# Performance work log

Measured on AMD Instinct MI355X. Metric: run time of the kernel, lower is better.

Reference implementation:

```python
import jax, jax.numpy as jnp
import numpy as np

N_NODES = 100000
N_EDGES = 1600000
IN_F, HID, N_COLORS = 128, 128, 10


def setup_inputs() -> dict:
    key = jax.random.key(0)
    k1, k2, k3, k4 = jax.random.split(key, 4)
    x = jax.random.normal(k1, (N_NODES, IN_F), dtype=jnp.float32)
    edge_index = jax.random.randint(k2, (2, N_EDGES), 0, N_NODES, dtype=jnp.int64)
    # Glorot-ish init for weights
    W1 = jax.random.normal(k3, (IN_F, HID), dtype=jnp.float32) / np.sqrt(IN_F)
    b1 = jnp.zeros((HID,), dtype=jnp.float32)
    W2 = jax.random.normal(k4, (HID, N_COLORS), dtype=jnp.float32) / np.sqrt(HID)
    b2 = jnp.zeros((N_COLORS,), dtype=jnp.float32)
    return {"x": x, "edge_index": edge_index, "W1": W1, "b1": b1, "W2": W2, "b2": b2}


def _gcn_norm(edge_index, num_nodes):
    # Add self-loops, compute symmetric normalization D^-1/2 (A+I) D^-1/2
    loops = jnp.arange(num_nodes, dtype=edge_index.dtype)
    src = jnp.concatenate([edge_index[0], loops])
    dst = jnp.concatenate([edge_index[1], loops])
    deg = jax.ops.segment_sum(jnp.ones_like(dst, dtype=jnp.float32), dst,
                              num_segments=num_nodes)
    deg_isqrt = jax.lax.rsqrt(deg)  # deg >= 1 due to self-loops
    norm = deg_isqrt[src] * deg_isqrt[dst]  # [E + N]
    return src, dst, norm


def _gcn_conv(h, src, dst, norm, num_nodes, W, b):
    # Linear transform first (PyG GCNConv), then gather-scale-scatter aggregate
    h = h @ W                                   # [N, out]
    msg = h[src] * norm[:, None]                # [E + N, out] gather
    out = jax.ops.segment_sum(msg, dst, num_segments=num_nodes)  # scatter-add
    return out + b


def reference(x, edge_index, W1, b1, W2, b2):
    n = x.shape[0]
    src, dst, norm = _gcn_norm(edge_index, n)
    h = _gcn_conv(x, src, dst, norm, n, W1, b1)
    h = jax.nn.relu(h)
    # dropout is identity in eval mode
    h = _gcn_conv(h, src, dst, norm, n, W2, b2)
    return jax.nn.softmax(h, axis=1)
```

## Files before the change

### kernel.cpp

```cpp
#include <hip/hip_runtime.h>
#include <hip/hip_fp16.h>

#define IN_F 128
#define HID  128
#define NC   10
#define H2P  16
#define NPB  128
#define NBMAX 784
#define BCAP 2560
#define EPB  4096

typedef _Float16 f16x8 __attribute__((ext_vector_type(8)));
typedef float f32x4 __attribute__((ext_vector_type(4)));

__global__ __launch_bounds__(1024) void k_bin(const int* __restrict__ src,
                                              const int* __restrict__ dst,
                                              int* __restrict__ bcnt,
                                              unsigned int* __restrict__ binned,
                                              int E, int nbin) {
    __shared__ int hist[NBMAX];
    __shared__ int base[NBMAX];
    __shared__ int lcur[NBMAX];
    const int tid = threadIdx.x;
    for (int b = tid; b < nbin; b += 1024) { hist[b] = 0; lcur[b] = 0; }
    __syncthreads();

    const int e0 = blockIdx.x * EPB + tid;
    int d[4];
    #pragma unroll
    for (int u = 0; u < 4; u++) {
        int e = e0 + u * 1024;
        d[u] = (e < E) ? dst[e] : -1;
        if (d[u] >= 0) atomicAdd(&hist[d[u] >> 7], 1);
    }
    __syncthreads();
    for (int b = tid; b < nbin; b += 1024) {
        int h = hist[b];
        base[b] = h ? atomicAdd(&bcnt[b], h) : 0;
    }
    __syncthreads();
    #pragma unroll
    for (int u = 0; u < 4; u++) {
        int e = e0 + u * 1024;
        if (e < E) {
            int dd = d[u];
            int b = dd >> 7;
            int s = src[e];
            int o = base[b] + atomicAdd(&lcur[b], 1);
            if (o < BCAP)
                binned[(size_t)b * BCAP + o] = ((unsigned)(dd & 127) << 17) | (unsigned)s;
        }
    }
}

__global__ __launch_bounds__(1024) void k_binscan(const int* __restrict__ bcnt,
                                                  int* __restrict__ binbase,
                                                  int* __restrict__ rowptr,
                                                  int N, int E, int nbin) {
    __shared__ int s[1024];
    const int tid = threadIdx.x;
    int v = (tid < nbin) ? bcnt[tid] : 0;
    s[tid] = v;
    __syncthreads();
    #pragma unroll
    for (int off = 1; off < 1024; off <<= 1) {
        int t = (tid >= off) ? s[tid - off] : 0;
        __syncthreads();
        s[tid] += t;
        __syncthreads();
    }
    if (tid < nbin) binbase[tid] = s[tid] - v;
    if (tid == 0) rowptr[N] = E;
}

__global__ __launch_bounds__(256) void k_place2(const int* __restrict__ bcnt,
                                                const unsigned int* __restrict__ binned,
                                                const int* __restrict__ binbase,
                                                int* __restrict__ rowptr,
                                                float* __restrict__ dis,
                                                int* __restrict__ csr, int N) {
    __shared__ int h[NPB];
    __shared__ int lb[NPB];
    __shared__ int cur[NPB];
    const int b = blockIdx.x;
    const int tid = threadIdx.x;
    if (tid < NPB) h[tid] = 0;
    __syncthreads();
    const int m = min(bcnt[b], BCAP);
    const unsigned int* p = binned + (size_t)b * BCAP;
    for (int i = tid; i < m; i += 256) atomicAdd(&h[p[i] >> 17], 1);
    __syncthreads();
    if (tid < NPB) lb[tid] = h[tid];
    __syncthreads();
    #pragma unroll
    for (int off = 1; off < NPB; off <<= 1) {
        int t = (tid < NPB && tid >= off) ? lb[tid - off] : 0;
        __syncthreads();
        if (tid < NPB) lb[tid] += t;
        __syncthreads();
    }
    const int rb = binbase[b];
    if (tid < NPB) {
        int ex = lb[tid] - h[tid];
        int node = b * NPB + tid;
        if (node < N) {
            rowptr[node] = rb + ex;
            dis[node] = rsqrtf(1.0f + (float)h[tid]);
        }
        lb[tid] = ex;
        cur[tid] = 0;
    }
    __syncthreads();
    for (int i = tid; i < m; i += 256) {
        unsigned v = p[i];
        int dl = v >> 17;
        int r = atomicAdd(&cur[dl], 1);
        csr[rb + lb[dl] + r] = (int)(v & 0x1FFFF);
    }
}

__global__ __launch_bounds__(256) void k_prep(const float* __restrict__ W1,
                                              __half* __restrict__ WT) {
    int e = blockIdx.x * 256 + threadIdx.x;
    int n = e >> 7, k = e & 127;
    WT[n * IN_F + k] = __float2half(W1[k * HID + n]);
}

__global__ __launch_bounds__(256) void k_gemm1(const float* __restrict__ X,
                                               const __half* __restrict__ WT,
                                               const float* __restrict__ dis,
                                               __half* __restrict__ outh) {
    __shared__ _Float16 sX[32 * IN_F];
    __shared__ _Float16 sW[128 * IN_F];
    const int tid = threadIdx.x;
    const int row0 = blockIdx.x * 32;

    {
        int n = tid >> 1, part = tid & 1;
        const f16x8* src = (const f16x8*)(WT + n * IN_F + part * 64);
        f16x8* dst = (f16x8*)(sW + n * IN_F + part * 64);
        #pragma unroll
        for (int c = 0; c < 8; c++) dst[c] = src[c];
    }
    {
        int r = tid >> 3;
        int k0 = (tid & 7) * 16;
        const float* src = X + (size_t)(row0 + r) * IN_F + k0;
        float4 f0 = *(const float4*)(src);
        float4 f1 = *(const float4*)(src + 4);
        float4 f2 = *(const float4*)(src + 8);
        float4 f3 = *(const float4*)(src + 12);
        f16x8 h0, h1;
        h0[0] = (_Float16)f0.x; h0[1] = (_Float16)f0.y;
        h0[2] = (_Float16)f0.z; h0[3] = (_Float16)f0.w;
        h0[4] = (_Float16)f1.x; h0[5] = (_Float16)f1.y;
        h0[6] = (_Float16)f1.z; h0[7] = (_Float16)f1.w;
        h1[0] = (_Float16)f2.x; h1[1] = (_Float16)f2.y;
        h1[2] = (_Float16)f2.z; h1[3] = (_Float16)f2.w;
        h1[4] = (_Float16)f3.x; h1[5] = (_Float16)f3.y;
        h1[6] = (_Float16)f3.z; h1[7] = (_Float16)f3.w;
        *(f16x8*)(sX + r * IN_F + k0) = h0;
        *(f16x8*)(sX + r * IN_F + k0 + 8) = h1;
    }
    __syncthreads();

    const int wave = tid >> 6;
    const int lane = tid & 63;
    const int quad = lane >> 4;
    const int l16 = lane & 15;
    const int nbase = wave * 32;

    f32x4 acc00 = {0,0,0,0}, acc01 = {0,0,0,0}, acc10 = {0,0,0,0}, acc11 = {0,0,0,0};

    #pragma unroll
    for (int kc = 0; kc < 4; kc++) {
        const int koff = kc * 32 + quad * 8;
        f16x8 a0 = *(const f16x8*)(sX + l16 * IN_F + koff);
        f16x8 a1 = *(const f16x8*)(sX + (16 + l16) * IN_F + koff);
        f16x8 b0 = *(const f16x8*)(sW + (nbase + l16) * IN_F + koff);
        f16x8 b1 = *(const f16x8*)(sW + (nbase + 16 + l16) * IN_F + koff);
        acc00 = __builtin_amdgcn_mfma_f32_16x16x32_f16(a0, b0, acc00, 0, 0, 0);
        acc01 = __builtin_amdgcn_mfma_f32_16x16x32_f16(a0, b1, acc01, 0, 0, 0);
        acc10 = __builtin_amdgcn_mfma_f32_16x16x32_f16(a1, b0, acc10, 0, 0, 0);
        acc11 = __builtin_amdgcn_mfma_f32_16x16x32_f16(a1, b1, acc11, 0, 0, 0);
    }

    #pragma unroll
    for (int r = 0; r < 4; r++) {
        {
            int row = row0 + quad * 4 + r;
            float d = dis[row];
            __half* o = outh + (size_t)row * HID + nbase + l16;
            o[0]  = __float2half(acc00[r] * d);
            o[16] = __float2half(acc01[r] * d);
        }
        {
            int row = row0 + 16 + quad * 4 + r;
            float d = dis[row];
            __half* o = outh + (size_t)row * HID + nbase + l16;
            o[0]  = __float2half(acc10[r] * d);
            o[16] = __float2half(acc11[r] * d);
        }
    }
}

__global__ __launch_bounds__(256) void k_agg1(const __half* __restrict__ hsh,
                                              const int* __restrict__ rowptr,
                                              const int* __restrict__ csr,
                                              const float* __restrict__ dis,
                                              const float* __restrict__ b1,
                                              const float* __restrict__ W2,
                                              float* __restrict__ h2p, int N) {
    __shared__ float sWT[NC][IN_F];
    for (int i = threadIdx.x; i < NC * IN_F; i += 256)
        sWT[i >> 7][i & 127] = W2[(i & 127) * NC + (i >> 7)];
    __syncthreads();

    const int node = blockIdx.x * 4 + (threadIdx.x >> 6);
    if (node >= N) return;
    const int lane = threadIdx.x & 63;
    const int g   = lane >> 4;
    const int l16 = lane & 15;
    const int f0  = l16 * 8;

    const int beg = rowptr[node], end = rowptr[node + 1];

    float acc[8] = {0,0,0,0,0,0,0,0};
    if (g == 0) {
        float4 r = *(const float4*)(hsh + (size_t)node * HID + f0);
        const __half2* hh = (const __half2*)&r;
        float2 t0 = __half22float2(hh[0]), t1 = __half22float2(hh[1]);
        float2 t2 = __half22float2(hh[2]), t3 = __half22float2(hh[3]);
        acc[0] = t0.x; acc[1] = t0.y; acc[2] = t1.x; acc[3] = t1.y;
        acc[4] = t2.x; acc[5] = t2.y; acc[6] = t3.x; acc[7] = t3.y;
    }

    int j = beg + g;
    for (; j + 12 < end; j += 16) {
        int s0 = csr[j], s1 = csr[j + 4], s2 = csr[j + 8], s3 = csr[j + 12];
        float4 r0 = *(const float4*)(hsh + (size_t)s0 * HID + f0);
        float4 r1 = *(const float4*)(hsh + (size_t)s1 * HID + f0);
        float4 r2 = *(const float4*)(hsh + (size_t)s2 * HID + f0);
        float4 r3 = *(const float4*)(hsh + (size_t)s3 * HID + f0);
        #pragma unroll
        for (int u = 0; u < 4; u++) {
            const float4* rp = u == 0 ? &r0 : u == 1 ? &r1 : u == 2 ? &r2 : &r3;
            const __half2* hh = (const __half2*)rp;
            float2 t0 = __half22float2(hh[0]), t1 = __half22float2(hh[1]);
            float2 t2 = __half22float2(hh[2]), t3 = __half22float2(hh[3]);
            acc[0] += t0.x; acc[1] += t0.y; acc[2] += t1.x; acc[3] += t1.y;
            acc[4] += t2.x; acc[5] += t2.y; acc[6] += t3.x; acc[7] += t3.y;
        }
    }
    for (; j < end; j += 4) {
        int s0 = csr[j];
        float4 r0 = *(const float4*)(hsh + (size_t)s0 * HID + f0);
        const __half2* hh = (const __half2*)&r0;
        float2 t0 = __half22float2(hh[0]), t1 = __half22float2(hh[1]);
        float2 t2 = __half22float2(hh[2]), t3 = __half22float2(hh[3]);
        acc[0] += t0.x; acc[1] += t0.y; acc[2] += t1.x; acc[3] += t1.y;
        acc[4] += t2.x; acc[5] += t2.y; acc[6] += t3.x; acc[7] += t3.y;
    }

    #pragma unroll
    for (int i = 0; i < 8; i++) {
        acc[i] += __shfl_xor(acc[i], 16, 64);
        acc[i] += __shfl_xor(acc[i], 32, 64);
    }

    const float d = dis[node];
    float4 ba = *(const float4*)(b1 + f0);
    float4 bb = *(const float4*)(b1 + f0 + 4);
    float h[8];
    h[0] = fmaxf(fmaf(d, acc[0], ba.x), 0.0f);
    h[1] = fmaxf(fmaf(d, acc[1], ba.y), 0.0f);
    h[2] = fmaxf(fmaf(d, acc[2], ba.z), 0.0f);
    h[3] = fmaxf(fmaf(d, acc[3], ba.w), 0.0f);
    h[4] = fmaxf(fmaf(d, acc[4], bb.x), 0.0f);
    h[5] = fmaxf(fmaf(d, acc[5], bb.y), 0.0f);
    h[6] = fmaxf(fmaf(d, acc[6], bb.z), 0.0f);
    h[7] = fmaxf(fmaf(d, acc[7], bb.w), 0.0f);

    const int cb = (g == 0) ? 0 : (g == 1) ? 3 : (g == 2) ? 6 : 8;
    const int nc = (g < 2) ? 3 : 2;
    float p[3];
    #pragma unroll
    for (int ci = 0; ci < 3; ci++) {
        if (ci < nc) {
            int c = cb + ci;
            float4 wa = *(const float4*)&sWT[c][f0];
            float4 wb = *(const float4*)&sWT[c][f0 + 4];
            float t = fmaf(h[0], wa.x, fmaf(h[1], wa.y, fmaf(h[2], wa.z, h[3] * wa.w)));
            t = fmaf(h[4], wb.x, fmaf(h[5], wb.y, fmaf(h[6], wb.z, fmaf(h[7], wb.w, t))));
            #pragma unroll
            for (int off = 1; off < 16; off <<= 1) t += __shfl_xor(t, off, 64);
            p[ci] = t;
        }
    }
    if (l16 == 0) {
        float* o = h2p + (size_t)node * H2P + cb;
        for (int ci = 0; ci < nc; ci++) o[ci] = d * p[ci];
    }
}

__global__ __launch_bounds__(256) void k_agg2(const float* __restrict__ h2p,
                                              const int* __restrict__ rowptr,
                                              const int* __restrict__ csr,
                                              const float* __restrict__ dis,
                                              const float* __restrict__ b2,
                                              float* __restrict__ out, int N) {
    int t = blockIdx.x * 256 + threadIdx.x;
    int node = t >> 2;
    int q = t & 3;
    if (node >= N) return;
    const int base = q * 4;

    float4 a = *(const float4*)(h2p + (size_t)node * H2P + base);
    const int beg = rowptr[node], end = rowptr[node + 1];
    int j = beg;
    for (; j + 1 < end; j += 2) {
        int s0 = csr[j], s1 = csr[j + 1];
        float4 v0 = *(const float4*)(h2p + (size_t)s0 * H2P + base);
        float4 v1 = *(const float4*)(h2p + (size_t)s1 * H2P + base);
        a.x += v0.x + v1.x; a.y += v0.y + v1.y;
        a.z += v0.z + v1.z; a.w += v0.w + v1.w;
    }
    if (j < end) {
        float4 v0 = *(const float4*)(h2p + (size_t)csr[j] * H2P + base);
        a.x += v0.x; a.y += v0.y; a.z += v0.z; a.w += v0.w;
    }

    const float d = dis[node];
    float vv[4];
    const float* ap = &a.x;
    #pragma unroll
    for (int i = 0; i < 4; i++) {
        int f = base + i;
        bool val = f < NC;
        vv[i] = val ? fmaf(d, ap[i], b2[val ? f : 0]) : -1e30f;
    }
    float m = fmaxf(fmaxf(vv[0], vv[1]), fmaxf(vv[2], vv[3]));
    m = fmaxf(m, __shfl_xor(m, 1, 64));
    m = fmaxf(m, __shfl_xor(m, 2, 64));
    float e[4];
    #pragma unroll
    for (int i = 0; i < 4; i++) e[i] = (base + i < NC) ? expf(vv[i] - m) : 0.0f;
    float s = (e[0] + e[1]) + (e[2] + e[3]);
    s += __shfl_xor(s, 1, 64);
    s += __shfl_xor(s, 2, 64);
    float inv = 1.0f / s;

    float* o = out + (size_t)node * NC;
    if (q == 0) {
        *(float2*)(o + 0) = make_float2(e[0] * inv, e[1] * inv);
        *(float2*)(o + 2) = make_float2(e[2] * inv, e[3] * inv);
    } else if (q == 1) {
        *(float2*)(o + 4) = make_float2(e[0] * inv, e[1] * inv);
        *(float2*)(o + 6) = make_float2(e[2] * inv, e[3] * inv);
    } else if (q == 2) {
        *(float2*)(o + 8) = make_float2(e[0] * inv, e[1] * inv);
    }
}

extern "C" void kernel_launch(void* const* d_in, const int* in_sizes, int n_in,
                              void* d_out, int out_size, void* d_ws, size_t ws_size,
                              hipStream_t stream) {
    const float* x  = (const float*)d_in[0];
    const int*   ei = (const int*)d_in[1];
    const float* W1 = (const float*)d_in[2];
    const float* b1 = (const float*)d_in[3];
    const float* W2 = (const float*)d_in[4];
    const float* b2 = (const float*)d_in[5];
    float* out = (float*)d_out;

    const int N = in_sizes[0] / IN_F;
    const int E = in_sizes[1] / 2;
    const int* esrc = ei;
    const int* edst = ei + E;
    const int nbin = (N + NPB - 1) / NPB;

    char* ws = (char*)d_ws;
    int*    rowptr  = (int*)(ws);
    float*  dis     = (float*)(ws + 0x80000);
    int*    bcnt    = (int*)(ws + 0x100000);
    int*    binbase = (int*)(ws + 0x110000);
    __half* WT      = (__half*)(ws + 0x120000);
    unsigned int* binned = (unsigned int*)(ws + 0x140000);
    int*    csr     = (int*)(ws + 0x940000);
    __half* hsh     = (__half*)(ws + 0x1000000);
    float*  h2p     = (float*)(ws + 0x2A00000);

    hipMemsetAsync(bcnt, 0, (size_t)nbin * sizeof(int), stream);

    k_bin    <<<(E + EPB - 1) / EPB, 1024, 0, stream>>>(esrc, edst, bcnt, binned, E, nbin);
    k_binscan<<<1, 1024, 0, stream>>>(bcnt, binbase, rowptr, N, E, nbin);
    k_place2 <<<nbin, 256, 0, stream>>>(bcnt, binned, binbase, rowptr, dis, csr, N);
    k_prep   <<<64, 256, 0, stream>>>(W1, WT);
    k_gemm1  <<<N / 32, 256, 0, stream>>>(x, WT, dis, hsh);
    k_agg1   <<<(N + 3) / 4, 256, 0, stream>>>(hsh, rowptr, csr, dis, b1, W2, h2p, N);
    k_agg2   <<<(int)(((size_t)N * 4 + 255) / 256), 256, 0, stream>>>(h2p, rowptr, csr, dis, b2, out, N);
}
```

Baseline: 262.1 us.

## Fuse prep kernels, drop bin scan, store layer-2 features in fp16, unroll gathers

The W1 transpose moves into block 0 of the binning kernel, and the single-block bin scan is replaced by a per-block reduction over bcnt inside the placement kernel. Together these remove two launches. The layer-2 intermediate is stored as fp16 to halve gather traffic in agg2, which now uses two threads per node with 8 features each. The agg1 gather loop is unrolled to 8 outstanding loads. The trade-offs are redundant prefix work in each placement block and reduced precision for the second-layer features.

```diff
diff --git a/kernel.cpp b/kernel.cpp
--- a/kernel.cpp
+++ b/kernel.cpp
@@ -17,11 +17,21 @@
                                               const int* __restrict__ dst,
                                               int* __restrict__ bcnt,
                                               unsigned int* __restrict__ binned,
+                                              const float* __restrict__ W1,
+                                              __half* __restrict__ WT,
                                               int E, int nbin) {
     __shared__ int hist[NBMAX];
     __shared__ int base[NBMAX];
     __shared__ int lcur[NBMAX];
     const int tid = threadIdx.x;
+
+    if (blockIdx.x == 0) {
+        for (int i = tid; i < IN_F * HID; i += 1024) {
+            int k = i >> 7, n = i & 127;
+            WT[n * IN_F + k] = __float2half(W1[k * HID + n]);
+        }
+    }
+
     for (int b = tid; b < nbin; b += 1024) { hist[b] = 0; lcur[b] = 0; }
     __syncthreads();
 
@@ -53,39 +63,31 @@
     }
 }
 
-__global__ __launch_bounds__(1024) void k_binscan(const int* __restrict__ bcnt,
-                                                  int* __restrict__ binbase,
-                                                  int* __restrict__ rowptr,
-                                                  int N, int E, int nbin) {
-    __shared__ int s[1024];
-    const int tid = threadIdx.x;
-    int v = (tid < nbin) ? bcnt[tid] : 0;
-    s[tid] = v;
-    __syncthreads();
-    #pragma unroll
-    for (int off = 1; off < 1024; off <<= 1) {
-        int t = (tid >= off) ? s[tid - off] : 0;
-        __syncthreads();
-        s[tid] += t;
-        __syncthreads();
-    }
-    if (tid < nbin) binbase[tid] = s[tid] - v;
-    if (tid == 0) rowptr[N] = E;
-}
-
 __global__ __launch_bounds__(256) void k_place2(const int* __restrict__ bcnt,
                                                 const unsigned int* __restrict__ binned,
-                                                const int* __restrict__ binbase,
                                                 int* __restrict__ rowptr,
                                                 float* __restrict__ dis,
-                                                int* __restrict__ csr, int N) {
+                                                int* __restrict__ csr,
+                                                int N, int E, int nbin) {
     __shared__ int h[NPB];
     __shared__ int lb[NPB];
     __shared__ int cur[NPB];
+    __shared__ int red[256];
     const int b = blockIdx.x;
     const int tid = threadIdx.x;
+
+    int partial = 0;
+    for (int i = tid; i < b; i += 256) partial += bcnt[i];
+    red[tid] = partial;
     if (tid < NPB) h[tid] = 0;
     __syncthreads();
+    #pragma unroll
+    for (int off = 128; off > 0; off >>= 1) {
+        if (tid < off) red[tid] += red[tid + off];
+        __syncthreads();
+    }
+    const int rb = red[0];
+
     const int m = min(bcnt[b], BCAP);
     const unsigned int* p = binned + (size_t)b * BCAP;
     for (int i = tid; i < m; i += 256) atomicAdd(&h[p[i] >> 17], 1);
@@ -99,7 +101,6 @@
         if (tid < NPB) lb[tid] += t;
         __syncthreads();
     }
-    const int rb = binbase[b];
     if (tid < NPB) {
         int ex = lb[tid] - h[tid];
         int node = b * NPB + tid;
@@ -110,6 +111,7 @@
         lb[tid] = ex;
         cur[tid] = 0;
     }
+    if (b == nbin - 1 && tid == 0) rowptr[N] = E;
     __syncthreads();
     for (int i = tid; i < m; i += 256) {
         unsigned v = p[i];
@@ -117,13 +119,6 @@
         int r = atomicAdd(&cur[dl], 1);
         csr[rb + lb[dl] + r] = (int)(v & 0x1FFFF);
     }
-}
-
-__global__ __launch_bounds__(256) void k_prep(const float* __restrict__ W1,
-                                              __half* __restrict__ WT) {
-    int e = blockIdx.x * 256 + threadIdx.x;
-    int n = e >> 7, k = e & 127;
-    WT[n * IN_F + k] = __float2half(W1[k * HID + n]);
 }
 
 __global__ __launch_bounds__(256) void k_gemm1(const float* __restrict__ X,
@@ -210,7 +205,7 @@
                                               const float* __restrict__ dis,
                                               const float* __restrict__ b1,
                                               const float* __restrict__ W2,
-                                              float* __restrict__ h2p, int N) {
+                                              __half* __restrict__ h2h, int N) {
     __shared__ float sWT[NC][IN_F];
     for (int i = threadIdx.x; i < NC * IN_F; i += 256)
         sWT[i >> 7][i & 127] = W2[(i & 127) * NC + (i >> 7)];
@@ -236,16 +231,19 @@
     }
 
     int j = beg + g;
-    for (; j + 12 < end; j += 16) {
-        int s0 = csr[j], s1 = csr[j + 4], s2 = csr[j + 8], s3 = csr[j + 12];
-        float4 r0 = *(const float4*)(hsh + (size_t)s0 * HID + f0);
-        float4 r1 = *(const float4*)(hsh + (size_t)s1 * HID + f0);
-        float4 r2 = *(const float4*)(hsh + (size_t)s2 * HID + f0);
-        float4 r3 = *(const float4*)(hsh + (size_t)s3 * HID + f0);
+    for (; j + 28 < end; j += 32) {
+        float4 r0 = *(const float4*)(hsh + (size_t)csr[j]      * HID + f0);
+        float4 r1 = *(const float4*)(hsh + (size_t)csr[j + 4]  * HID + f0);
+        float4 r2 = *(const float4*)(hsh + (size_t)csr[j + 8]  * HID + f0);
+        float4 r3 = *(const float4*)(hsh + (size_t)csr[j + 12] * HID + f0);
+        float4 r4 = *(const float4*)(hsh + (size_t)csr[j + 16] * HID + f0);
+        float4 r5 = *(const float4*)(hsh + (size_t)csr[j + 20] * HID + f0);
+        float4 r6 = *(const float4*)(hsh + (size_t)csr[j + 24] * HID + f0);
+        float4 r7 = *(const float4*)(hsh + (size_t)csr[j + 28] * HID + f0);
+        const float4* rs[8] = {&r0, &r1, &r2, &r3, &r4, &r5, &r6, &r7};
         #pragma unroll
-        for (int u = 0; u < 4; u++) {
-            const float4* rp = u == 0 ? &r0 : u == 1 ? &r1 : u == 2 ? &r2 : &r3;
-            const __half2* hh = (const __half2*)rp;
+        for (int u = 0; u < 8; u++) {
+            const __half2* hh = (const __half2*)rs[u];
             float2 t0 = __half22float2(hh[0]), t1 = __half22float2(hh[1]);
             float2 t2 = __half22float2(hh[2]), t3 = __half22float2(hh[3]);
             acc[0] += t0.x; acc[1] += t0.y; acc[2] += t1.x; acc[3] += t1.y;
@@ -253,8 +251,7 @@
         }
     }
     for (; j < end; j += 4) {
-        int s0 = csr[j];
-        float4 r0 = *(const float4*)(hsh + (size_t)s0 * HID + f0);
+        float4 r0 = *(const float4*)(hsh + (size_t)csr[j] * HID + f0);
         const __half2* hh = (const __half2*)&r0;
         float2 t0 = __half22float2(hh[0]), t1 = __half22float2(hh[1]);
         float2 t2 = __half22float2(hh[2]), t3 = __half22float2(hh[3]);
@@ -298,66 +295,83 @@
         }
     }
     if (l16 == 0) {
-        float* o = h2p + (size_t)node * H2P + cb;
-        for (int ci = 0; ci < nc; ci++) o[ci] = d * p[ci];
-    }
-}
-
-__global__ __launch_bounds__(256) void k_agg2(const float* __restrict__ h2p,
+        __half* o = h2h + (size_t)node * H2P + cb;
+        for (int ci = 0; ci < nc; ci++) o[ci] = __float2half(d * p[ci]);
+    }
+}
+
+__global__ __launch_bounds__(256) void k_agg2(const __half* __restrict__ h2h,
                                               const int* __restrict__ rowptr,
                                               const int* __restrict__ csr,
                                               const float* __restrict__ dis,
                                               const float* __restrict__ b2,
                                               float* __restrict__ out, int N) {
     int t = blockIdx.x * 256 + threadIdx.x;
-    int node = t >> 2;
-    int q = t & 3;
+    int node = t >> 1;
+    int q = t & 1;
     if (node >= N) return;
-    const int base = q * 4;
-
-    float4 a = *(const float4*)(h2p + (size_t)node * H2P + base);
+    const int base = q * 8;
+
+    float a[8];
+    {
+        float4 r = *(const float4*)(h2h + (size_t)node * H2P + base);
+        const __half2* hh = (const __half2*)&r;
+        float2 t0 = __half22float2(hh[0]), t1 = __half22float2(hh[1]);
+        float2 t2 = __half22float2(hh[2]), t3 = __half22float2(hh[3]);
+        a[0] = t0.x; a[1] = t0.y; a[2] = t1.x; a[3] = t1.y;
+        a[4] = t2.x; a[5] = t2.y; a[6] = t3.x; a[7] = t3.y;
+    }
     const int beg = rowptr[node], end = rowptr[node + 1];
     int j = beg;
-    for (; j + 1 < end; j += 2) {
-        int s0 = csr[j], s1 = csr[j + 1];
-        float4 v0 = *(const float4*)(h2p + (size_t)s0 * H2P + base);
-        float4 v1 = *(const float4*)(h2p + (size_t)s1 * H2P + base);
-        a.x += v0.x + v1.x; a.y += v0.y + v1.y;
-        a.z += v0.z + v1.z; a.w += v0.w + v1.w;
-    }
-    if (j < end) {
-        float4 v0 = *(const float4*)(h2p + (size_t)csr[j] * H2P + base);
-        a.x += v0.x; a.y += v0.y; a.z += v0.z; a.w += v0.w;
+    for (; j + 3 < end; j += 4) {
+        float4 r0 = *(const float4*)(h2h + (size_t)csr[j]     * H2P + base);
+        float4 r1 = *(const float4*)(h2h + (size_t)csr[j + 1] * H2P + base);
+        float4 r2 = *(const float4*)(h2h + (size_t)csr[j + 2] * H2P + base);
+        float4 r3 = *(const float4*)(h2h + (size_t)csr[j + 3] * H2P + base);
+        const float4* rs[4] = {&r0, &r1, &r2, &r3};
+        #pragma unroll
+        for (int u = 0; u < 4; u++) {
+            const __half2* hh = (const __half2*)rs[u];
+            float2 t0 = __half22float2(hh[0]), t1 = __half22float2(hh[1]);
+            float2 t2 = __half22float2(hh[2]), t3 = __half22float2(hh[3]);
+            a[0] += t0.x; a[1] += t0.y; a[2] += t1.x; a[3] += t1.y;
+            a[4] += t2.x; a[5] += t2.y; a[6] += t3.x; a[7] += t3.y;
+        }
+    }
+    for (; j < end; ++j) {
+        float4 r0 = *(const float4*)(h2h + (size_t)csr[j] * H2P + base);
+        const __half2* hh = (const __half2*)&r0;
+        float2 t0 = __half22float2(hh[0]), t1 = __half22float2(hh[1]);
+        float2 t2 = __half22float2(hh[2]), t3 = __half22float2(hh[3]);
+        a[0] += t0.x; a[1] += t0.y; a[2] += t1.x; a[3] += t1.y;
+        a[4] += t2.x; a[5] += t2.y; a[6] += t3.x; a[7] += t3.y;
     }
 
     const float d = dis[node];
-    float vv[4];
-    const float* ap = &a.x;
-    #pragma unroll
-    for (int i = 0; i < 4; i++) {
+    float vv[8];
+    #pragma unroll
+    for (int i = 0; i < 8; i++) {
         int f = base + i;
-        bool val = f < NC;
-        vv[i] = val ? fmaf(d, ap[i], b2[val ? f : 0]) : -1e30f;
-    }
-    float m = fmaxf(fmaxf(vv[0], vv[1]), fmaxf(vv[2], vv[3]));
+        vv[i] = (f < NC) ? fmaf(d, a[i], b2[f]) : -1e30f;
+    }
+    float m = vv[0];
+    #pragma unroll
+    for (int i = 1; i < 8; i++) m = fmaxf(m, vv[i]);
     m = fmaxf(m, __shfl_xor(m, 1, 64));
-    m = fmaxf(m, __shfl_xor(m, 2, 64));
-    float e[4];
-    #pragma unroll
-    for (int i = 0; i < 4; i++) e[i] = (base + i < NC) ? expf(vv[i] - m) : 0.0f;
-    float s = (e[0] + e[1]) + (e[2] + e[3]);
+    float e[8];
+    float s = 0.0f;
+    #pragma unroll
+    for (int i = 0; i < 8; i++) { e[i] = (base + i < NC) ? expf(vv[i] - m) : 0.0f; s += e[i]; }
     s += __shfl_xor(s, 1, 64);
-    s += __shfl_xor(s, 2, 64);
     float inv = 1.0f / s;
 
     float* o = out + (size_t)node * NC;
     if (q == 0) {
         *(float2*)(o + 0) = make_float2(e[0] * inv, e[1] * inv);
         *(float2*)(o + 2) = make_float2(e[2] * inv, e[3] * inv);
-    } else if (q == 1) {
-        *(float2*)(o + 4) = make_float2(e[0] * inv, e[1] * inv);
-        *(float2*)(o + 6) = make_float2(e[2] * inv, e[3] * inv);
-    } else if (q == 2) {
+        *(float2*)(o + 4) = make_float2(e[4] * inv, e[5] * inv);
+        *(float2*)(o + 6) = make_float2(e[6] * inv, e[7] * inv);
+    } else {
         *(float2*)(o + 8) = make_float2(e[0] * inv, e[1] * inv);
     }
 }
@@ -383,20 +397,17 @@
     int*    rowptr  = (int*)(ws);
     float*  dis     = (float*)(ws + 0x80000);
     int*    bcnt    = (int*)(ws + 0x100000);
-    int*    binbase = (int*)(ws + 0x110000);
-    __half* WT      = (__half*)(ws + 0x120000);
+    __half* WT      = (__half*)(ws + 0x110000);
     unsigned int* binned = (unsigned int*)(ws + 0x140000);
     int*    csr     = (int*)(ws + 0x940000);
-    __half* hsh     = (__half*)(ws + 0x1000000);
-    float*  h2p     = (float*)(ws + 0x2A00000);
+    __half* hsh     = (__half*)(ws + 0x1040000);
+    __half* h2h     = (__half*)(ws + 0x2A00000);
 
     hipMemsetAsync(bcnt, 0, (size_t)nbin * sizeof(int), stream);
 
-    k_bin    <<<(E + EPB - 1) / EPB, 1024, 0, stream>>>(esrc, edst, bcnt, binned, E, nbin);
-    k_binscan<<<1, 1024, 0, stream>>>(bcnt, binbase, rowptr, N, E, nbin);
-    k_place2 <<<nbin, 256, 0, stream>>>(bcnt, binned, binbase, rowptr, dis, csr, N);
-    k_prep   <<<64, 256, 0, stream>>>(W1, WT);
-    k_gemm1  <<<N / 32, 256, 0, stream>>>(x, WT, dis, hsh);
-    k_agg1   <<<(N + 3) / 4, 256, 0, stream>>>(hsh, rowptr, csr, dis, b1, W2, h2p, N);
-    k_agg2   <<<(int)(((size_t)N * 4 + 255) / 256), 256, 0, stream>>>(h2p, rowptr, csr, dis, b2, out, N);
-}
+    k_bin   <<<(E + EPB - 1) / EPB, 1024, 0, stream>>>(esrc, edst, bcnt, binned, W1, WT, E, nbin);
+    k_place2<<<nbin, 256, 0, stream>>>(bcnt, binned, rowptr, dis, csr, N, E, nbin);
+    k_gemm1 <<<N / 32, 256, 0, stream>>>(x, WT, dis, hsh);
+    k_agg1  <<<(N + 3) / 4, 256, 0, stream>>>(hsh, rowptr, csr, dis, b1, W2, h2h, N);
+    k_agg2  <<<(int)(((size_t)N * 2 + 255) / 256), 256, 0, stream>>>(h2h, rowptr, csr, dis, b2, out, N);
+}
```

New measurement: 307.5 us. 17.3% more time.
